# Performance work log

Measured on AMD Instinct MI355X. Metric: run time of the kernel, lower is better.

The kernel has to match this reference:

```python
import jax, jax.numpy as jnp
import numpy as np

N = 10000      # nodes
E = 320000     # edges (avg degree 32)
C = 256        # feature dim (input_dim == output_dim)
L = 3          # num_layers
D = 20         # KAF dictionary size
BOUNDARY = 4.0 # KAF dictionary boundary


def setup_inputs() -> dict:
    key = jax.random.key(0)
    ks = jax.random.split(key, 7)
    x = jax.random.normal(ks[0], (N, C), jnp.float32)
    edge_index = jax.random.randint(ks[1], (2, E), 0, N, jnp.int32)
    edge_attr = jax.random.normal(ks[2], (E, 2), jnp.float32)
    # per-layer stacked parameters (all layers have identical shapes)
    node_w = jax.random.normal(ks[3], (L, C, C), jnp.float32) / jnp.sqrt(jnp.float32(C))
    edge_w = jax.random.normal(ks[4], (L, 2, C), jnp.float32) / jnp.sqrt(jnp.float32(2))
    neigh_w = jax.random.normal(ks[5], (L, C, C), jnp.float32) / jnp.sqrt(jnp.float32(C))
    bias = jnp.zeros((L, C), jnp.float32)
    alpha = jax.random.normal(ks[6], (L, C, D), jnp.float32) * 0.3
    return dict(x=x, edge_index=edge_index, edge_attr=edge_attr,
                node_w=node_w, edge_w=edge_w, neigh_w=neigh_w, bias=bias, alpha=alpha)


def _kaf(s, alpha_l):
    # Kernel Activation Function (Scardapane et al.): per-channel Gaussian mixture
    dict_pts = jnp.linspace(-BOUNDARY, BOUNDARY, D, dtype=s.dtype)  # [D]
    interval = 2.0 * BOUNDARY / (D - 1)
    gamma = 0.5 / (2.0 * interval) ** 2
    K = jnp.exp(-gamma * jnp.square(s[..., None] - dict_pts))  # [N, C, D]
    return jnp.einsum('ncd,cd->nc', K, alpha_l)


def reference(x, edge_index, edge_attr, node_w, edge_w, neigh_w, bias, alpha):
    src, dst = edge_index[0], edge_index[1]
    # mean-aggregation normalizer (computed once; graph is fixed across layers)
    cnt = jax.ops.segment_sum(jnp.ones((E,), x.dtype), dst, num_segments=N)
    inv_cnt = jnp.where(cnt > 0, 1.0 / jnp.maximum(cnt, 1.0), 0.0)  # [N]
    h = x
    for l in range(L):
        # message: edge_attr @ W_e + x_j @ W_n  -> [E, C]
        msg = edge_attr @ edge_w[l] + h[src] @ neigh_w[l]
        # mean aggregate to destination nodes
        aggr = jax.ops.segment_sum(msg, dst, num_segments=N) * inv_cnt[:, None]
        # update: KAF(aggr + x @ W + b)
        h = _kaf(aggr + h @ node_w[l] + bias[l], alpha[l])
    return h
```

## Files before the change

kernel.cpp:

```cpp
#include <hip/hip_runtime.h>
#include <hip/hip_bf16.h>

#define N_NODES 10000
#define N_EDGES 320000
#define B_PRE   80
#define EPB     (N_EDGES / B_PRE)
#define SLK     130

typedef __attribute__((ext_vector_type(8))) _Float16 half8;
typedef __attribute__((ext_vector_type(4))) _Float16 half4;
typedef __attribute__((ext_vector_type(4))) float floatx4;

#define OFF_RS    0
#define OFF_INVC  40960
#define OFF_S2    81920
#define OFF_COLV  163840
#define OFF_WCAT  806912
#define OFF_HA    1593344
#define OFF_HB    6713344
#define OFF_G     11833344
#define OFF_PERC  OFF_G
#define OFF_BASE  (OFF_G + 1600000)
#define OFF_CTOT  (OFF_G + 4800000)
#define OFF_EA2   OFF_HB

__global__ __launch_bounds__(256) void k_prep(const float4* __restrict__ x, half4* __restrict__ hA,
                                              const float* __restrict__ neigh_w, const float* __restrict__ node_w,
                                              _Float16* __restrict__ wcatT) {
  __shared__ float t[32][33];
  const int b = blockIdx.x;
  if (b < 2500) {
    int i = b * 256 + threadIdx.x;
    float4 v = x[i];
    half4 h; h.x = (_Float16)v.x; h.y = (_Float16)v.y; h.z = (_Float16)v.z; h.w = (_Float16)v.w;
    hA[i] = h;
    return;
  }
  const int bb = b - 2500;
  const int k0 = (bb & 15) * 32;
  const int n0 = ((bb >> 4) & 7) * 32;
  const int l  = bb >> 7;
  const int tx = threadIdx.x & 31;
  const int ty = threadIdx.x >> 5;
  const float* src = (k0 < 256) ? neigh_w : node_w;
  const int kb = (k0 < 256) ? k0 : (k0 - 256);
#pragma unroll
  for (int p = 0; p < 4; ++p) {
    int k = kb + ty + p * 8;
    t[ty + p * 8][tx] = src[l * 65536 + k * 256 + (n0 + tx)];
  }
  __syncthreads();
#pragma unroll
  for (int p = 0; p < 4; ++p) {
    int n = n0 + ty + p * 8;
    wcatT[(size_t)l * 131072 + n * 512 + (k0 + tx)] = (_Float16)t[tx][ty + p * 8];
  }
}

__global__ __launch_bounds__(1024) void k_count(const int* __restrict__ ei,
                                                unsigned short* __restrict__ percnt) {
  __shared__ int hist[N_NODES];
  const int t = threadIdx.x, b = blockIdx.x;
  for (int n = t; n < N_NODES; n += 1024) hist[n] = 0;
  __syncthreads();
  const int e0 = b * EPB;
  for (int e = e0 + t; e < e0 + EPB; e += 1024)
    atomicAdd(&hist[ei[N_EDGES + e]], 1);
  __syncthreads();
  for (int n = t; n < N_NODES; n += 1024)
    percnt[b * N_NODES + n] = (unsigned short)hist[n];
}

__global__ __launch_bounds__(256) void k_base(const unsigned short* __restrict__ percnt,
                                              int* __restrict__ prefix, int* __restrict__ cnttot) {
  int n = blockIdx.x * 256 + threadIdx.x;
  if (n >= N_NODES) return;
  int s = 0;
  for (int b = 0; b < B_PRE; ++b) {
    prefix[b * N_NODES + n] = s;
    s += (int)percnt[b * N_NODES + n];
  }
  cnttot[n] = s;
}

__global__ __launch_bounds__(1024) void k_scan(const int* __restrict__ cnttot,
                                               int* __restrict__ rs, float* __restrict__ invc) {
  __shared__ int lds[1024];
  const int t = threadIdx.x;
  const int base = t * 10;
  int loc[10];
  int sum = 0;
#pragma unroll
  for (int i = 0; i < 10; ++i) {
    int idx = base + i;
    int v = (idx < N_NODES) ? cnttot[idx] : 0;
    loc[i] = v; sum += v;
  }
  lds[t] = sum; __syncthreads();
  for (int off = 1; off < 1024; off <<= 1) {
    int v = 0;
    if (t >= off) v = lds[t - off];
    __syncthreads();
    if (t >= off) lds[t] += v;
    __syncthreads();
  }
  int ex = lds[t] - sum;
#pragma unroll
  for (int i = 0; i < 10; ++i) {
    int idx = base + i;
    if (idx < N_NODES) {
      rs[idx] = ex; ex += loc[i];
      invc[idx] = (loc[i] > 0) ? (1.0f / (float)loc[i]) : 0.0f;
    }
  }
  if (t == 1023) rs[N_NODES] = lds[1023];
}

__global__ __launch_bounds__(1024) void k_scat(const int* __restrict__ ei, const float* __restrict__ ea,
                                               const int* __restrict__ prefix, const int* __restrict__ rs,
                                               unsigned short* __restrict__ colv, float2* __restrict__ ea2) {
  __shared__ int cur[N_NODES];
  const int t = threadIdx.x, b = blockIdx.x;
  for (int n = t; n < N_NODES; n += 1024)
    cur[n] = rs[n] + prefix[b * N_NODES + n];
  __syncthreads();
  const int e0 = b * EPB;
  for (int e = e0 + t; e < e0 + EPB; e += 1024) {
    int d = ei[N_EDGES + e];
    int src = ei[e];
    float2 a = ((const float2*)ea)[e];
    int pos = atomicAdd(&cur[d], 1);
    colv[pos] = (unsigned short)src;
    ea2[pos] = a;
  }
}

__global__ __launch_bounds__(256) void k_s2(const int* __restrict__ rs, const float2* __restrict__ ea2,
                                            float* __restrict__ s2) {
  int n = blockIdx.x * 256 + threadIdx.x;
  if (n >= N_NODES) return;
  int beg = rs[n], end = rs[n + 1];
  float sx = 0.f, sy = 0.f;
  for (int p = beg; p < end; ++p) { float2 a = ea2[p]; sx += a.x; sy += a.y; }
  s2[2 * n] = sx; s2[2 * n + 1] = sy;
}

__global__ __launch_bounds__(256) void k_aggr(const int* __restrict__ rs, const unsigned short* __restrict__ colv,
                                              const float* __restrict__ invc,
                                              const _Float16* __restrict__ H, _Float16* __restrict__ Gm) {
  const int wv   = threadIdx.x >> 6;
  const int lane = threadIdx.x & 63;
  const int hf   = lane >> 5;
  const int l5   = lane & 31;
  const int n = blockIdx.x * 4 + wv;
  int beg = rs[n], end = rs[n + 1];
  beg = max(0, min(beg, N_EDGES));
  end = max(beg, min(end, N_EDGES));
  const int co = l5 * 8;

  half8 acc0 = (half8)(_Float16)0.f, acc1 = (half8)(_Float16)0.f;
  half8 acc2 = (half8)(_Float16)0.f, acc3 = (half8)(_Float16)0.f;
  for (int base = beg; base < end; base += 64) {
    const int cnt = min(64, end - base);
    int myIdx = 0;
    if (base + lane < end) myIdx = (int)colv[base + lane];
    int j = 0;
    for (; j + 8 <= cnt; j += 8) {
      int s0 = __shfl(myIdx, j + hf);
      int s1 = __shfl(myIdx, j + 2 + hf);
      int s2i = __shfl(myIdx, j + 4 + hf);
      int s3 = __shfl(myIdx, j + 6 + hf);
      half8 v0 = *(const half8*)(H + (size_t)s0 * 256 + co);
      half8 v1 = *(const half8*)(H + (size_t)s1 * 256 + co);
      half8 v2 = *(const half8*)(H + (size_t)s2i * 256 + co);
      half8 v3 = *(const half8*)(H + (size_t)s3 * 256 + co);
      acc0 += v0; acc1 += v1; acc2 += v2; acc3 += v3;
    }
    for (; j + 2 <= cnt; j += 2) {
      int s0 = __shfl(myIdx, j + hf);
      acc0 += *(const half8*)(H + (size_t)s0 * 256 + co);
    }
    if (j < cnt) {
      int s0 = __shfl(myIdx, j);
      if (hf == 0)
        acc0 += *(const half8*)(H + (size_t)s0 * 256 + co);
    }
  }
  acc0 = (acc0 + acc2) + (acc1 + acc3);
  union { half8 h; unsigned int u[4]; } me, ot;
  me.h = acc0;
#pragma unroll
  for (int r = 0; r < 4; ++r) ot.u[r] = (unsigned int)__shfl_xor((int)me.u[r], 32);
  acc0 = me.h + ot.h;

  if (hf == 0) {
    const float ic = invc[n];
    half8 o;
#pragma unroll
    for (int k = 0; k < 8; ++k) o[k] = (_Float16)((float)acc0[k] * ic);
    *(half8*)(Gm + (size_t)n * 256 + co) = o;
  }
}

__global__ __launch_bounds__(256) void k_gemm2(const _Float16* __restrict__ Gm,
                                               const _Float16* __restrict__ Hm,
                                               const _Float16* __restrict__ BT,
                                               const float* __restrict__ ew,
                                               const float* __restrict__ bias,
                                               const float* __restrict__ alpha,
                                               const float* __restrict__ invc,
                                               const float* __restrict__ s2,
                                               _Float16* __restrict__ hout, float* __restrict__ fout,
                                               int final_layer) {
  __shared__ _Float16 As[64 * SLK];
  __shared__ _Float16 Bs[64 * SLK];
  __shared__ float alds[64 * 20];
  const int tid = threadIdx.x;
  const int wv = tid >> 6;
  const int lane = tid & 63;
  const int m0 = blockIdx.x * 64;
  const int n0 = blockIdx.y * 64;
  const int wy = wv >> 1, wx = wv & 1;

#pragma unroll
  for (int ii = 0; ii < 5; ++ii)
    alds[tid + 256 * ii] = alpha[n0 * 20 + tid + 256 * ii];

  floatx4 acc[2][2];
#pragma unroll
  for (int i = 0; i < 2; ++i)
#pragma unroll
    for (int j = 0; j < 2; ++j) acc[i][j] = (floatx4){0.f, 0.f, 0.f, 0.f};

  const int mrow = 32 * wy + (lane & 15);
  const int nrow = 32 * wx + (lane & 15);
  const int q8 = (lane >> 4) * 8;

#pragma unroll
  for (int kt = 0; kt < 4; ++kt) {
    const _Float16* Asrc = (kt < 2) ? Gm : Hm;
    const int ko = (kt & 1) * 128;
    half8 av[4], bv[4];
#pragma unroll
    for (int c = 0; c < 4; ++c) {
      int ch = tid + 256 * c;
      int row = ch >> 4;
      int off = (ch & 15) * 8;
      int arow = m0 + row; if (arow >= N_NODES) arow = N_NODES - 1;
      av[c] = *(const half8*)(Asrc + (size_t)arow * 256 + ko + off);
      bv[c] = *(const half8*)(BT + (size_t)(n0 + row) * 512 + kt * 128 + off);
    }
    __syncthreads();
#pragma unroll
    for (int c = 0; c < 4; ++c) {
      int ch = tid + 256 * c;
      int row = ch >> 4;
      int off = (ch & 15) * 8;
      *(half8*)&As[row * SLK + off] = av[c];
      *(half8*)&Bs[row * SLK + off] = bv[c];
    }
    __syncthreads();
#pragma unroll
    for (int ks = 0; ks < 4; ++ks) {
      const int kb = ks * 32 + q8;
      half8 af0 = *(const half8*)&As[mrow * SLK + kb];
      half8 af1 = *(const half8*)&As[(mrow + 16) * SLK + kb];
      half8 bf0 = *(const half8*)&Bs[nrow * SLK + kb];
      half8 bf1 = *(const half8*)&Bs[(nrow + 16) * SLK + kb];
      acc[0][0] = __builtin_amdgcn_mfma_f32_16x16x32_f16(af0, bf0, acc[0][0], 0, 0, 0);
      acc[0][1] = __builtin_amdgcn_mfma_f32_16x16x32_f16(af0, bf1, acc[0][1], 0, 0, 0);
      acc[1][0] = __builtin_amdgcn_mfma_f32_16x16x32_f16(af1, bf0, acc[1][0], 0, 0, 0);
      acc[1][1] = __builtin_amdgcn_mfma_f32_16x16x32_f16(af1, bf1, acc[1][1], 0, 0, 0);
    }
  }

  const int rowb = m0 + 32 * wy + 4 * (lane >> 4);
  const int clb  = 32 * wx + (lane & 15);
  float icr[2][4], t0r[2][4], t1r[2][4];
#pragma unroll
  for (int i = 0; i < 2; ++i)
#pragma unroll
    for (int r = 0; r < 4; ++r) {
      int rw = rowb + 16 * i + r;
      int rc = (rw < N_NODES) ? rw : (N_NODES - 1);
      icr[i][r] = invc[rc];
      t0r[i][r] = s2[2 * rc];
      t1r[i][r] = s2[2 * rc + 1];
    }
  const float WM = 0.7788007831f;
#pragma unroll
  for (int j = 0; j < 2; ++j) {
    const int cl = clb + 16 * j;
    const int cn = n0 + cl;
    const float e0 = ew[cn], e1 = ew[256 + cn], bi = bias[cn];
    float a20[20];
#pragma unroll
    for (int q = 0; q < 5; ++q)
      *(float4*)&a20[4 * q] = *(const float4*)&alds[cl * 20 + 4 * q];
#pragma unroll
    for (int i = 0; i < 2; ++i) {
      float K[4], R[4], o[4];
#pragma unroll
      for (int r = 0; r < 4; ++r) {
        float sv = acc[i][j][r] + icr[i][r] * (t0r[i][r] * e0 + t1r[i][r] * e1) + bi;
        float tt = fminf(fmaxf(sv, -40.f), 40.f);
        float dd = tt + 4.0f;
        K[r] = __expf(-0.705078125f * dd * dd);
        R[r] = __expf(0.59375f * dd - 0.125f);
        o[r] = 0.f;
      }
#pragma unroll
      for (int d = 0; d < 20; ++d) {
        o[0] += a20[d] * K[0]; K[0] *= R[0]; R[0] *= WM;
        o[1] += a20[d] * K[1]; K[1] *= R[1]; R[1] *= WM;
        o[2] += a20[d] * K[2]; K[2] *= R[2]; R[2] *= WM;
        o[3] += a20[d] * K[3]; K[3] *= R[3]; R[3] *= WM;
      }
      const int rw0 = rowb + 16 * i;
      if (final_layer) {
#pragma unroll
        for (int r = 0; r < 4; ++r)
          if (rw0 + r < N_NODES) fout[(size_t)(rw0 + r) * 256 + cn] = o[r];
      } else {
#pragma unroll
        for (int r = 0; r < 4; ++r)
          if (rw0 + r < N_NODES) hout[(size_t)(rw0 + r) * 256 + cn] = (_Float16)o[r];
      }
    }
  }
}

extern "C" void kernel_launch(void* const* d_in, const int* in_sizes, int n_in,
                              void* d_out, int out_size, void* d_ws, size_t ws_size,
                              hipStream_t stream) {
  const float* x       = (const float*)d_in[0];
  const int*   ei      = (const int*)d_in[1];
  const float* ea      = (const float*)d_in[2];
  const float* node_w  = (const float*)d_in[3];
  const float* edge_w  = (const float*)d_in[4];
  const float* neigh_w = (const float*)d_in[5];
  const float* bias    = (const float*)d_in[6];
  const float* alpha   = (const float*)d_in[7];

  char* w = (char*)d_ws;
  int*            rs     = (int*)(w + OFF_RS);
  float*          invc   = (float*)(w + OFF_INVC);
  float*          s2     = (float*)(w + OFF_S2);
  unsigned short* colv   = (unsigned short*)(w + OFF_COLV);
  _Float16*       wcatT  = (_Float16*)(w + OFF_WCAT);
  _Float16*       hA     = (_Float16*)(w + OFF_HA);
  _Float16*       hB     = (_Float16*)(w + OFF_HB);
  _Float16*       g      = (_Float16*)(w + OFF_G);
  unsigned short* percnt = (unsigned short*)(w + OFF_PERC);
  int*            prefix = (int*)(w + OFF_BASE);
  int*            cnttot = (int*)(w + OFF_CTOT);
  float2*         ea2    = (float2*)(w + OFF_EA2);
  float*          fout   = (float*)d_out;

  k_prep<<<2884, 256, 0, stream>>>((const float4*)x, (half4*)hA, neigh_w, node_w, wcatT);
  k_count<<<B_PRE, 1024, 0, stream>>>(ei, percnt);
  k_base<<<40, 256, 0, stream>>>(percnt, prefix, cnttot);
  k_scan<<<1, 1024, 0, stream>>>(cnttot, rs, invc);
  k_scat<<<B_PRE, 1024, 0, stream>>>(ei, ea, prefix, rs, colv, ea2);
  k_s2<<<40, 256, 0, stream>>>(rs, ea2, s2);

  _Float16* hin = hA;
  for (int l = 0; l < 3; ++l) {
    k_aggr<<<2500, 256, 0, stream>>>(rs, colv, invc, hin, g);
    _Float16* hout = (l == 0) ? hB : hA;
    k_gemm2<<<dim3(157, 4), 256, 0, stream>>>(g, hin, wcatT + (size_t)l * 131072,
                                              edge_w + l * 512, bias + l * 256, alpha + l * 5120,
                                              invc, s2, hout, fout, (l == 2) ? 1 : 0);
    hin = hout;
  }
}
```

Measured before the change: 213.3 us.

## Fuse CSR preprocessing kernels into one cooperative kernel with grid syncs

Merges the six preprocessing kernels (fp16 cast, weight transpose, histogram, prefix, scan, scatter, edge-attr sums) into a single cooperative launch of 80 blocks that uses grid.sync between phases. The aim is to remove five kernel launch gaps and their inter-kernel drain. In exchange, the elementwise cast and transpose run on only 80 blocks instead of thousands, and each grid barrier has its own cost, so the lower parallelism may offset part of the launch savings.

```diff
diff --git a/kernel.cpp b/kernel.cpp
--- a/kernel.cpp
+++ b/kernel.cpp
@@ -1,5 +1,8 @@
 #include <hip/hip_runtime.h>
 #include <hip/hip_bf16.h>
+#include <hip/hip_cooperative_groups.h>
+
+namespace cg = cooperative_groups;
 
 #define N_NODES 10000
 #define N_EDGES 320000
@@ -24,125 +27,117 @@
 #define OFF_CTOT  (OFF_G + 4800000)
 #define OFF_EA2   OFF_HB
 
-__global__ __launch_bounds__(256) void k_prep(const float4* __restrict__ x, half4* __restrict__ hA,
+__global__ __launch_bounds__(1024) void k_pre(const float4* __restrict__ x, half4* __restrict__ hA,
                                               const float* __restrict__ neigh_w, const float* __restrict__ node_w,
-                                              _Float16* __restrict__ wcatT) {
+                                              _Float16* __restrict__ wcatT,
+                                              const int* __restrict__ ei, const float* __restrict__ ea,
+                                              unsigned short* __restrict__ percnt, int* __restrict__ prefix,
+                                              int* __restrict__ cnttot, int* __restrict__ rs,
+                                              float* __restrict__ invc, unsigned short* __restrict__ colv,
+                                              float2* __restrict__ ea2, float* __restrict__ s2) {
+  cg::grid_group grid = cg::this_grid();
+  __shared__ int hist[N_NODES];
   __shared__ float t[32][33];
-  const int b = blockIdx.x;
-  if (b < 2500) {
-    int i = b * 256 + threadIdx.x;
+  __shared__ int slds[1024];
+  const int tid = threadIdx.x, b = blockIdx.x;
+  const int gtid = b * 1024 + tid;
+
+  for (int n = tid; n < N_NODES; n += 1024) hist[n] = 0;
+
+  for (int i = gtid; i < 640000; i += 81920) {
     float4 v = x[i];
     half4 h; h.x = (_Float16)v.x; h.y = (_Float16)v.y; h.z = (_Float16)v.z; h.w = (_Float16)v.w;
     hA[i] = h;
-    return;
-  }
-  const int bb = b - 2500;
-  const int k0 = (bb & 15) * 32;
-  const int n0 = ((bb >> 4) & 7) * 32;
-  const int l  = bb >> 7;
-  const int tx = threadIdx.x & 31;
-  const int ty = threadIdx.x >> 5;
-  const float* src = (k0 < 256) ? neigh_w : node_w;
-  const int kb = (k0 < 256) ? k0 : (k0 - 256);
-#pragma unroll
-  for (int p = 0; p < 4; ++p) {
-    int k = kb + ty + p * 8;
-    t[ty + p * 8][tx] = src[l * 65536 + k * 256 + (n0 + tx)];
-  }
+  }
+
   __syncthreads();
-#pragma unroll
-  for (int p = 0; p < 4; ++p) {
-    int n = n0 + ty + p * 8;
-    wcatT[(size_t)l * 131072 + n * 512 + (k0 + tx)] = (_Float16)t[tx][ty + p * 8];
-  }
-}
-
-__global__ __launch_bounds__(1024) void k_count(const int* __restrict__ ei,
-                                                unsigned short* __restrict__ percnt) {
-  __shared__ int hist[N_NODES];
-  const int t = threadIdx.x, b = blockIdx.x;
-  for (int n = t; n < N_NODES; n += 1024) hist[n] = 0;
-  __syncthreads();
+  for (int tile = b; tile < 384; tile += 80) {
+    const int k0 = (tile & 15) * 32;
+    const int n0 = ((tile >> 4) & 7) * 32;
+    const int l  = tile >> 7;
+    const int r = tid >> 5, c = tid & 31;
+    const float* src = (k0 < 256) ? neigh_w : node_w;
+    const int kb = (k0 < 256) ? k0 : (k0 - 256);
+    t[r][c] = src[l * 65536 + (kb + r) * 256 + (n0 + c)];
+    __syncthreads();
+    wcatT[(size_t)l * 131072 + (n0 + r) * 512 + (k0 + c)] = (_Float16)t[c][r];
+    __syncthreads();
+  }
+
   const int e0 = b * EPB;
-  for (int e = e0 + t; e < e0 + EPB; e += 1024)
+  for (int e = e0 + tid; e < e0 + EPB; e += 1024)
     atomicAdd(&hist[ei[N_EDGES + e]], 1);
   __syncthreads();
-  for (int n = t; n < N_NODES; n += 1024)
+  for (int n = tid; n < N_NODES; n += 1024)
     percnt[b * N_NODES + n] = (unsigned short)hist[n];
-}
-
-__global__ __launch_bounds__(256) void k_base(const unsigned short* __restrict__ percnt,
-                                              int* __restrict__ prefix, int* __restrict__ cnttot) {
-  int n = blockIdx.x * 256 + threadIdx.x;
-  if (n >= N_NODES) return;
-  int s = 0;
-  for (int b = 0; b < B_PRE; ++b) {
-    prefix[b * N_NODES + n] = s;
-    s += (int)percnt[b * N_NODES + n];
-  }
-  cnttot[n] = s;
-}
-
-__global__ __launch_bounds__(1024) void k_scan(const int* __restrict__ cnttot,
-                                               int* __restrict__ rs, float* __restrict__ invc) {
-  __shared__ int lds[1024];
-  const int t = threadIdx.x;
-  const int base = t * 10;
-  int loc[10];
-  int sum = 0;
-#pragma unroll
-  for (int i = 0; i < 10; ++i) {
-    int idx = base + i;
-    int v = (idx < N_NODES) ? cnttot[idx] : 0;
-    loc[i] = v; sum += v;
-  }
-  lds[t] = sum; __syncthreads();
-  for (int off = 1; off < 1024; off <<= 1) {
-    int v = 0;
-    if (t >= off) v = lds[t - off];
-    __syncthreads();
-    if (t >= off) lds[t] += v;
-    __syncthreads();
-  }
-  int ex = lds[t] - sum;
-#pragma unroll
-  for (int i = 0; i < 10; ++i) {
-    int idx = base + i;
-    if (idx < N_NODES) {
-      rs[idx] = ex; ex += loc[i];
-      invc[idx] = (loc[i] > 0) ? (1.0f / (float)loc[i]) : 0.0f;
-    }
-  }
-  if (t == 1023) rs[N_NODES] = lds[1023];
-}
-
-__global__ __launch_bounds__(1024) void k_scat(const int* __restrict__ ei, const float* __restrict__ ea,
-                                               const int* __restrict__ prefix, const int* __restrict__ rs,
-                                               unsigned short* __restrict__ colv, float2* __restrict__ ea2) {
-  __shared__ int cur[N_NODES];
-  const int t = threadIdx.x, b = blockIdx.x;
-  for (int n = t; n < N_NODES; n += 1024)
-    cur[n] = rs[n] + prefix[b * N_NODES + n];
+
+  grid.sync();
+
+  if (tid < 125) {
+    const int n = b * 125 + tid;
+    int s = 0;
+    for (int bb = 0; bb < B_PRE; ++bb) {
+      prefix[bb * N_NODES + n] = s;
+      s += (int)percnt[bb * N_NODES + n];
+    }
+    cnttot[n] = s;
+  }
+
+  grid.sync();
+
+  if (b == 0) {
+    const int base = tid * 10;
+    int loc[10];
+    int sum = 0;
+#pragma unroll
+    for (int i = 0; i < 10; ++i) {
+      int idx = base + i;
+      int v = (idx < N_NODES) ? cnttot[idx] : 0;
+      loc[i] = v; sum += v;
+    }
+    slds[tid] = sum; __syncthreads();
+    for (int off = 1; off < 1024; off <<= 1) {
+      int v = 0;
+      if (tid >= off) v = slds[tid - off];
+      __syncthreads();
+      if (tid >= off) slds[tid] += v;
+      __syncthreads();
+    }
+    int ex = slds[tid] - sum;
+#pragma unroll
+    for (int i = 0; i < 10; ++i) {
+      int idx = base + i;
+      if (idx < N_NODES) {
+        rs[idx] = ex; ex += loc[i];
+        invc[idx] = (loc[i] > 0) ? (1.0f / (float)loc[i]) : 0.0f;
+      }
+    }
+    if (tid == 1023) rs[N_NODES] = slds[1023];
+  }
+
+  grid.sync();
+
+  for (int n = tid; n < N_NODES; n += 1024)
+    hist[n] = rs[n] + prefix[b * N_NODES + n];
   __syncthreads();
-  const int e0 = b * EPB;
-  for (int e = e0 + t; e < e0 + EPB; e += 1024) {
+  for (int e = e0 + tid; e < e0 + EPB; e += 1024) {
     int d = ei[N_EDGES + e];
-    int src = ei[e];
+    int srcn = ei[e];
     float2 a = ((const float2*)ea)[e];
-    int pos = atomicAdd(&cur[d], 1);
-    colv[pos] = (unsigned short)src;
+    int pos = atomicAdd(&hist[d], 1);
+    colv[pos] = (unsigned short)srcn;
     ea2[pos] = a;
   }
-}
-
-__global__ __launch_bounds__(256) void k_s2(const int* __restrict__ rs, const float2* __restrict__ ea2,
-                                            float* __restrict__ s2) {
-  int n = blockIdx.x * 256 + threadIdx.x;
-  if (n >= N_NODES) return;
-  int beg = rs[n], end = rs[n + 1];
-  float sx = 0.f, sy = 0.f;
-  for (int p = beg; p < end; ++p) { float2 a = ea2[p]; sx += a.x; sy += a.y; }
-  s2[2 * n] = sx; s2[2 * n + 1] = sy;
+
+  grid.sync();
+
+  if (tid < 125) {
+    const int n = b * 125 + tid;
+    int beg = rs[n], end = rs[n + 1];
+    float sx = 0.f, sy = 0.f;
+    for (int p = beg; p < end; ++p) { float2 a = ea2[p]; sx += a.x; sy += a.y; }
+    s2[2 * n] = sx; s2[2 * n + 1] = sy;
+  }
 }
 
 __global__ __launch_bounds__(256) void k_aggr(const int* __restrict__ rs, const unsigned short* __restrict__ colv,
@@ -357,12 +352,12 @@
   float2*         ea2    = (float2*)(w + OFF_EA2);
   float*          fout   = (float*)d_out;
 
-  k_prep<<<2884, 256, 0, stream>>>((const float4*)x, (half4*)hA, neigh_w, node_w, wcatT);
-  k_count<<<B_PRE, 1024, 0, stream>>>(ei, percnt);
-  k_base<<<40, 256, 0, stream>>>(percnt, prefix, cnttot);
-  k_scan<<<1, 1024, 0, stream>>>(cnttot, rs, invc);
-  k_scat<<<B_PRE, 1024, 0, stream>>>(ei, ea, prefix, rs, colv, ea2);
-  k_s2<<<40, 256, 0, stream>>>(rs, ea2, s2);
+  const float4* x4  = (const float4*)x;
+  half4*        hA4 = (half4*)hA;
+  void* kargs[] = { (void*)&x4, (void*)&hA4, (void*)&neigh_w, (void*)&node_w, (void*)&wcatT,
+                    (void*)&ei, (void*)&ea, (void*)&percnt, (void*)&prefix, (void*)&cnttot,
+                    (void*)&rs, (void*)&invc, (void*)&colv, (void*)&ea2, (void*)&s2 };
+  hipLaunchCooperativeKernel((const void*)k_pre, dim3(B_PRE), dim3(1024), kargs, 0, stream);
 
   _Float16* hin = hA;
   for (int l = 0; l < 3; ++l) {
```

Result: slower. 273.7 us (+28.3%).

## Fuse neighbor aggregation into GEMM+KAF kernel via shared-memory G tile

Applied to the files above, without the earlier changes.

Merges the separate aggregation kernel and the GEMM/KAF kernel into one kernel per layer. Each 512-thread block gathers and averages 32 nodes' neighbor features into LDS, then runs MFMA over the full 256 output columns, reading B fragments and the H-half of A straight from global memory. This removes the global round-trip of the aggregated G matrix and one launch per layer. In exchange it uses only 313 blocks, which means lower parallelism for the latency-bound gather phase, and it drops LDS staging for the weight tiles.

```diff
diff --git a/kernel.cpp b/kernel.cpp
--- a/kernel.cpp
+++ b/kernel.cpp
@@ -5,7 +5,7 @@
 #define N_EDGES 320000
 #define B_PRE   80
 #define EPB     (N_EDGES / B_PRE)
-#define SLK     130
+#define SG      258
 
 typedef __attribute__((ext_vector_type(8))) _Float16 half8;
 typedef __attribute__((ext_vector_type(4))) _Float16 half4;
@@ -18,10 +18,10 @@
 #define OFF_WCAT  806912
 #define OFF_HA    1593344
 #define OFF_HB    6713344
-#define OFF_G     11833344
-#define OFF_PERC  OFF_G
-#define OFF_BASE  (OFF_G + 1600000)
-#define OFF_CTOT  (OFF_G + 4800000)
+#define OFF_SCR   11833344
+#define OFF_PERC  OFF_SCR
+#define OFF_BASE  (OFF_SCR + 1600000)
+#define OFF_CTOT  (OFF_SCR + 4800000)
 #define OFF_EA2   OFF_HB
 
 __global__ __launch_bounds__(256) void k_prep(const float4* __restrict__ x, half4* __restrict__ hA,
@@ -145,187 +145,151 @@
   s2[2 * n] = sx; s2[2 * n + 1] = sy;
 }
 
-__global__ __launch_bounds__(256) void k_aggr(const int* __restrict__ rs, const unsigned short* __restrict__ colv,
-                                              const float* __restrict__ invc,
-                                              const _Float16* __restrict__ H, _Float16* __restrict__ Gm) {
-  const int wv   = threadIdx.x >> 6;
-  const int lane = threadIdx.x & 63;
+__global__ __launch_bounds__(512) void k_gat(const int* __restrict__ rs, const unsigned short* __restrict__ colv,
+                                             const float* __restrict__ invc, const float* __restrict__ s2v,
+                                             const _Float16* __restrict__ H,
+                                             const _Float16* __restrict__ BT,
+                                             const float* __restrict__ ew,
+                                             const float* __restrict__ bias,
+                                             const float* __restrict__ alpha,
+                                             _Float16* __restrict__ hout, float* __restrict__ fout,
+                                             int final_layer) {
+  __shared__ _Float16 Gs[32 * SG];
+  __shared__ float alds[256 * 20];
+  const int tid  = threadIdx.x;
+  const int wv   = tid >> 6;
+  const int lane = tid & 63;
   const int hf   = lane >> 5;
   const int l5   = lane & 31;
-  const int n = blockIdx.x * 4 + wv;
-  int beg = rs[n], end = rs[n + 1];
-  beg = max(0, min(beg, N_EDGES));
-  end = max(beg, min(end, N_EDGES));
+  const int m0   = blockIdx.x * 32;
+
+#pragma unroll
+  for (int i = 0; i < 10; ++i) alds[tid + 512 * i] = alpha[tid + 512 * i];
+
   const int co = l5 * 8;
-
-  half8 acc0 = (half8)(_Float16)0.f, acc1 = (half8)(_Float16)0.f;
-  half8 acc2 = (half8)(_Float16)0.f, acc3 = (half8)(_Float16)0.f;
-  for (int base = beg; base < end; base += 64) {
-    const int cnt = min(64, end - base);
-    int myIdx = 0;
-    if (base + lane < end) myIdx = (int)colv[base + lane];
-    int j = 0;
-    for (; j + 8 <= cnt; j += 8) {
-      int s0 = __shfl(myIdx, j + hf);
-      int s1 = __shfl(myIdx, j + 2 + hf);
-      int s2i = __shfl(myIdx, j + 4 + hf);
-      int s3 = __shfl(myIdx, j + 6 + hf);
-      half8 v0 = *(const half8*)(H + (size_t)s0 * 256 + co);
-      half8 v1 = *(const half8*)(H + (size_t)s1 * 256 + co);
-      half8 v2 = *(const half8*)(H + (size_t)s2i * 256 + co);
-      half8 v3 = *(const half8*)(H + (size_t)s3 * 256 + co);
-      acc0 += v0; acc1 += v1; acc2 += v2; acc3 += v3;
-    }
-    for (; j + 2 <= cnt; j += 2) {
-      int s0 = __shfl(myIdx, j + hf);
-      acc0 += *(const half8*)(H + (size_t)s0 * 256 + co);
-    }
-    if (j < cnt) {
-      int s0 = __shfl(myIdx, j);
-      if (hf == 0)
-        acc0 += *(const half8*)(H + (size_t)s0 * 256 + co);
-    }
-  }
-  acc0 = (acc0 + acc2) + (acc1 + acc3);
-  union { half8 h; unsigned int u[4]; } me, ot;
-  me.h = acc0;
-#pragma unroll
-  for (int r = 0; r < 4; ++r) ot.u[r] = (unsigned int)__shfl_xor((int)me.u[r], 32);
-  acc0 = me.h + ot.h;
-
-  if (hf == 0) {
-    const float ic = invc[n];
-    half8 o;
-#pragma unroll
-    for (int k = 0; k < 8; ++k) o[k] = (_Float16)((float)acc0[k] * ic);
-    *(half8*)(Gm + (size_t)n * 256 + co) = o;
-  }
-}
-
-__global__ __launch_bounds__(256) void k_gemm2(const _Float16* __restrict__ Gm,
-                                               const _Float16* __restrict__ Hm,
-                                               const _Float16* __restrict__ BT,
-                                               const float* __restrict__ ew,
-                                               const float* __restrict__ bias,
-                                               const float* __restrict__ alpha,
-                                               const float* __restrict__ invc,
-                                               const float* __restrict__ s2,
-                                               _Float16* __restrict__ hout, float* __restrict__ fout,
-                                               int final_layer) {
-  __shared__ _Float16 As[64 * SLK];
-  __shared__ _Float16 Bs[64 * SLK];
-  __shared__ float alds[64 * 20];
-  const int tid = threadIdx.x;
-  const int wv = tid >> 6;
-  const int lane = tid & 63;
-  const int m0 = blockIdx.x * 64;
-  const int n0 = blockIdx.y * 64;
-  const int wy = wv >> 1, wx = wv & 1;
-
-#pragma unroll
-  for (int ii = 0; ii < 5; ++ii)
-    alds[tid + 256 * ii] = alpha[n0 * 20 + tid + 256 * ii];
-
-  floatx4 acc[2][2];
-#pragma unroll
-  for (int i = 0; i < 2; ++i)
-#pragma unroll
-    for (int j = 0; j < 2; ++j) acc[i][j] = (floatx4){0.f, 0.f, 0.f, 0.f};
-
-  const int mrow = 32 * wy + (lane & 15);
-  const int nrow = 32 * wx + (lane & 15);
+  for (int it = 0; it < 4; ++it) {
+    const int r = wv * 4 + it;
+    int n = m0 + r; if (n > N_NODES - 1) n = N_NODES - 1;
+    int beg = rs[n], end = rs[n + 1];
+    beg = max(0, min(beg, N_EDGES));
+    end = max(beg, min(end, N_EDGES));
+
+    half8 acc0 = (half8)(_Float16)0.f, acc1 = (half8)(_Float16)0.f;
+    half8 acc2 = (half8)(_Float16)0.f, acc3 = (half8)(_Float16)0.f;
+    for (int base = beg; base < end; base += 64) {
+      const int cnt = min(64, end - base);
+      int myIdx = 0;
+      if (base + lane < end) myIdx = (int)colv[base + lane];
+      int j = 0;
+      for (; j + 8 <= cnt; j += 8) {
+        int i0 = __shfl(myIdx, j + hf);
+        int i1 = __shfl(myIdx, j + 2 + hf);
+        int i2 = __shfl(myIdx, j + 4 + hf);
+        int i3 = __shfl(myIdx, j + 6 + hf);
+        half8 v0 = *(const half8*)(H + (size_t)i0 * 256 + co);
+        half8 v1 = *(const half8*)(H + (size_t)i1 * 256 + co);
+        half8 v2 = *(const half8*)(H + (size_t)i2 * 256 + co);
+        half8 v3 = *(const half8*)(H + (size_t)i3 * 256 + co);
+        acc0 += v0; acc1 += v1; acc2 += v2; acc3 += v3;
+      }
+      for (; j + 2 <= cnt; j += 2) {
+        int i0 = __shfl(myIdx, j + hf);
+        acc0 += *(const half8*)(H + (size_t)i0 * 256 + co);
+      }
+      if (j < cnt) {
+        int i0 = __shfl(myIdx, j);
+        if (hf == 0)
+          acc0 += *(const half8*)(H + (size_t)i0 * 256 + co);
+      }
+    }
+    acc0 = (acc0 + acc2) + (acc1 + acc3);
+    union { half8 h; unsigned int u[4]; } me, ot;
+    me.h = acc0;
+#pragma unroll
+    for (int q = 0; q < 4; ++q) ot.u[q] = (unsigned int)__shfl_xor((int)me.u[q], 32);
+    acc0 = me.h + ot.h;
+
+    if (hf == 0) {
+      const float ic = invc[n];
+      half8 o;
+#pragma unroll
+      for (int k = 0; k < 8; ++k) o[k] = (_Float16)((float)acc0[k] * ic);
+      *(half8*)&Gs[r * SG + co] = o;
+    }
+  }
+  __syncthreads();
+
+  const int wy = wv >> 2;
+  const int wx = wv & 3;
+  const int ml = lane & 15;
   const int q8 = (lane >> 4) * 8;
+  const int am = 16 * wy + ml;
+  const int ag = (m0 + am < N_NODES) ? (m0 + am) : (N_NODES - 1);
+
+  floatx4 acc[4];
+#pragma unroll
+  for (int nt = 0; nt < 4; ++nt) acc[nt] = (floatx4){0.f, 0.f, 0.f, 0.f};
 
 #pragma unroll
   for (int kt = 0; kt < 4; ++kt) {
-    const _Float16* Asrc = (kt < 2) ? Gm : Hm;
-    const int ko = (kt & 1) * 128;
-    half8 av[4], bv[4];
-#pragma unroll
-    for (int c = 0; c < 4; ++c) {
-      int ch = tid + 256 * c;
-      int row = ch >> 4;
-      int off = (ch & 15) * 8;
-      int arow = m0 + row; if (arow >= N_NODES) arow = N_NODES - 1;
-      av[c] = *(const half8*)(Asrc + (size_t)arow * 256 + ko + off);
-      bv[c] = *(const half8*)(BT + (size_t)(n0 + row) * 512 + kt * 128 + off);
-    }
-    __syncthreads();
-#pragma unroll
-    for (int c = 0; c < 4; ++c) {
-      int ch = tid + 256 * c;
-      int row = ch >> 4;
-      int off = (ch & 15) * 8;
-      *(half8*)&As[row * SLK + off] = av[c];
-      *(half8*)&Bs[row * SLK + off] = bv[c];
-    }
-    __syncthreads();
 #pragma unroll
     for (int ks = 0; ks < 4; ++ks) {
-      const int kb = ks * 32 + q8;
-      half8 af0 = *(const half8*)&As[mrow * SLK + kb];
-      half8 af1 = *(const half8*)&As[(mrow + 16) * SLK + kb];
-      half8 bf0 = *(const half8*)&Bs[nrow * SLK + kb];
-      half8 bf1 = *(const half8*)&Bs[(nrow + 16) * SLK + kb];
-      acc[0][0] = __builtin_amdgcn_mfma_f32_16x16x32_f16(af0, bf0, acc[0][0], 0, 0, 0);
-      acc[0][1] = __builtin_amdgcn_mfma_f32_16x16x32_f16(af0, bf1, acc[0][1], 0, 0, 0);
-      acc[1][0] = __builtin_amdgcn_mfma_f32_16x16x32_f16(af1, bf0, acc[1][0], 0, 0, 0);
-      acc[1][1] = __builtin_amdgcn_mfma_f32_16x16x32_f16(af1, bf1, acc[1][1], 0, 0, 0);
-    }
-  }
-
-  const int rowb = m0 + 32 * wy + 4 * (lane >> 4);
-  const int clb  = 32 * wx + (lane & 15);
-  float icr[2][4], t0r[2][4], t1r[2][4];
-#pragma unroll
-  for (int i = 0; i < 2; ++i)
-#pragma unroll
-    for (int r = 0; r < 4; ++r) {
-      int rw = rowb + 16 * i + r;
-      int rc = (rw < N_NODES) ? rw : (N_NODES - 1);
-      icr[i][r] = invc[rc];
-      t0r[i][r] = s2[2 * rc];
-      t1r[i][r] = s2[2 * rc + 1];
-    }
+      const int kk = ks * 32 + q8;
+      half8 af;
+      if (kt < 2) af = *(const half8*)&Gs[am * SG + kt * 128 + kk];
+      else        af = *(const half8*)(H + (size_t)ag * 256 + (kt - 2) * 128 + kk);
+#pragma unroll
+      for (int nt = 0; nt < 4; ++nt) {
+        const int nb = 64 * wx + 16 * nt + ml;
+        half8 bf = *(const half8*)(BT + (size_t)nb * 512 + kt * 128 + kk);
+        acc[nt] = __builtin_amdgcn_mfma_f32_16x16x32_f16(af, bf, acc[nt], 0, 0, 0);
+      }
+    }
+  }
+
+  const int rowb = m0 + 16 * wy + 4 * (lane >> 4);
+  float icr[4], t0r[4], t1r[4];
+#pragma unroll
+  for (int r = 0; r < 4; ++r) {
+    int rc = (rowb + r < N_NODES) ? (rowb + r) : (N_NODES - 1);
+    icr[r] = invc[rc];
+    t0r[r] = s2v[2 * rc];
+    t1r[r] = s2v[2 * rc + 1];
+  }
   const float WM = 0.7788007831f;
 #pragma unroll
-  for (int j = 0; j < 2; ++j) {
-    const int cl = clb + 16 * j;
-    const int cn = n0 + cl;
+  for (int nt = 0; nt < 4; ++nt) {
+    const int cn = 64 * wx + 16 * nt + ml;
     const float e0 = ew[cn], e1 = ew[256 + cn], bi = bias[cn];
     float a20[20];
 #pragma unroll
     for (int q = 0; q < 5; ++q)
-      *(float4*)&a20[4 * q] = *(const float4*)&alds[cl * 20 + 4 * q];
-#pragma unroll
-    for (int i = 0; i < 2; ++i) {
-      float K[4], R[4], o[4];
-#pragma unroll
-      for (int r = 0; r < 4; ++r) {
-        float sv = acc[i][j][r] + icr[i][r] * (t0r[i][r] * e0 + t1r[i][r] * e1) + bi;
-        float tt = fminf(fmaxf(sv, -40.f), 40.f);
-        float dd = tt + 4.0f;
-        K[r] = __expf(-0.705078125f * dd * dd);
-        R[r] = __expf(0.59375f * dd - 0.125f);
-        o[r] = 0.f;
-      }
-#pragma unroll
-      for (int d = 0; d < 20; ++d) {
-        o[0] += a20[d] * K[0]; K[0] *= R[0]; R[0] *= WM;
-        o[1] += a20[d] * K[1]; K[1] *= R[1]; R[1] *= WM;
-        o[2] += a20[d] * K[2]; K[2] *= R[2]; R[2] *= WM;
-        o[3] += a20[d] * K[3]; K[3] *= R[3]; R[3] *= WM;
-      }
-      const int rw0 = rowb + 16 * i;
-      if (final_layer) {
-#pragma unroll
-        for (int r = 0; r < 4; ++r)
-          if (rw0 + r < N_NODES) fout[(size_t)(rw0 + r) * 256 + cn] = o[r];
-      } else {
-#pragma unroll
-        for (int r = 0; r < 4; ++r)
-          if (rw0 + r < N_NODES) hout[(size_t)(rw0 + r) * 256 + cn] = (_Float16)o[r];
-      }
+      *(float4*)&a20[4 * q] = *(const float4*)&alds[cn * 20 + 4 * q];
+    float K[4], R[4], o[4];
+#pragma unroll
+    for (int r = 0; r < 4; ++r) {
+      float sv = acc[nt][r] + icr[r] * (t0r[r] * e0 + t1r[r] * e1) + bi;
+      float tt = fminf(fmaxf(sv, -40.f), 40.f);
+      float dd = tt + 4.0f;
+      K[r] = __expf(-0.705078125f * dd * dd);
+      R[r] = __expf(0.59375f * dd - 0.125f);
+      o[r] = 0.f;
+    }
+#pragma unroll
+    for (int d = 0; d < 20; ++d) {
+      o[0] += a20[d] * K[0]; K[0] *= R[0]; R[0] *= WM;
+      o[1] += a20[d] * K[1]; K[1] *= R[1]; R[1] *= WM;
+      o[2] += a20[d] * K[2]; K[2] *= R[2]; R[2] *= WM;
+      o[3] += a20[d] * K[3]; K[3] *= R[3]; R[3] *= WM;
+    }
+    if (final_layer) {
+#pragma unroll
+      for (int r = 0; r < 4; ++r)
+        if (rowb + r < N_NODES) fout[(size_t)(rowb + r) * 256 + cn] = o[r];
+    } else {
+#pragma unroll
+      for (int r = 0; r < 4; ++r)
+        if (rowb + r < N_NODES) hout[(size_t)(rowb + r) * 256 + cn] = (_Float16)o[r];
     }
   }
 }
@@ -350,7 +314,6 @@
   _Float16*       wcatT  = (_Float16*)(w + OFF_WCAT);
   _Float16*       hA     = (_Float16*)(w + OFF_HA);
   _Float16*       hB     = (_Float16*)(w + OFF_HB);
-  _Float16*       g      = (_Float16*)(w + OFF_G);
   unsigned short* percnt = (unsigned short*)(w + OFF_PERC);
   int*            prefix = (int*)(w + OFF_BASE);
   int*            cnttot = (int*)(w + OFF_CTOT);
@@ -366,11 +329,10 @@
 
   _Float16* hin = hA;
   for (int l = 0; l < 3; ++l) {
-    k_aggr<<<2500, 256, 0, stream>>>(rs, colv, invc, hin, g);
     _Float16* hout = (l == 0) ? hB : hA;
-    k_gemm2<<<dim3(157, 4), 256, 0, stream>>>(g, hin, wcatT + (size_t)l * 131072,
-                                              edge_w + l * 512, bias + l * 256, alpha + l * 5120,
-                                              invc, s2, hout, fout, (l == 2) ? 1 : 0);
+    k_gat<<<313, 512, 0, stream>>>(rs, colv, invc, s2, hin, wcatT + (size_t)l * 131072,
+                                   edge_w + l * 512, bias + l * 256, alpha + l * 5120,
+                                   hout, fout, (l == 2) ? 1 : 0);
     hin = hout;
   }
 }
```

Result: slower. 287.9 us (+35.0%).
